# Performance work log

Measured on AMD Instinct MI355X. Metric: run time of the kernel, lower is better.

## Reference

```python
import math
import jax, jax.numpy as jnp
import numpy as np

B, N1, N2 = 4, 1024, 768
DIM, H, DK = 1536, 8, 64
DV = DIM // H          # 192
NRPF = DIM // H        # 192, divisible by 6
ESM_CELL = 1280 + 256  # 1536
LN_EPS = 1e-5


def layer_norm(t, g, b):
    mu = jnp.mean(t, axis=-1, keepdims=True)
    var = jnp.mean(jnp.square(t - mu), axis=-1, keepdims=True)
    return (t - mu) * jax.lax.rsqrt(var + LN_EPS) * g + b


def positional_embed(n, feature_size):
    # Enformer-style relative positional features for distances -n+1..n-1
    distances = jnp.arange(-n + 1, n, dtype=jnp.float32)  # [2n-1]
    absd = jnp.abs(distances)[:, None]
    nb = feature_size // 6  # 3 basis fns x 2 (sym + signed)
    seq_len = float(n)
    # exponential
    max_range = math.log(seq_len) / math.log(2.0)
    half_life = 2.0 ** jnp.linspace(3.0, max_range, nb)
    f_exp = jnp.exp(-math.log(2.0) / half_life * absd)
    # central mask
    widths = 2.0 ** jnp.arange(1, nb + 1, dtype=jnp.float32) - 1.0
    f_cm = (widths[None, :] > absd).astype(jnp.float32)
    # gamma pdf
    stddev = seq_len / (2.0 * nb)
    start_mean = seq_len / nb
    mean = jnp.linspace(start_mean, seq_len, nb)
    conc = (mean / stddev) ** 2
    rate = mean / stddev ** 2
    log_p = jax.scipy.special.xlogy(conc - 1.0, absd) - rate * absd
    log_norm = jax.scipy.special.gammaln(conc) - conc * jnp.log(rate)
    prob = jnp.exp(log_p - log_norm) + 1e-8
    f_gam = prob / jnp.max(prob, axis=-1, keepdims=True)
    emb = jnp.concatenate([f_exp, f_cm, f_gam], axis=-1)
    return jnp.concatenate([emb, jnp.sign(distances)[:, None] * emb], axis=-1)  # [2n-1, feature_size]


def relative_shift(x):
    # x: [b, h, t1, 2n-1] -> [b, h, t1, n]
    b, h, t1, _ = x.shape
    x = jnp.pad(x, ((0, 0), (0, 0), (0, 0), (1, 0)))
    t2 = x.shape[-1]  # 2n
    x = x.reshape(b, h, t2, t1)[:, :, 1:, :].reshape(b, h, t1, t2 - 1)
    return x[..., : (t2 + 1) // 2]


def ffn(t, g, b, w1, b1, w2, b2):
    h = layer_norm(t, g, b)
    h = jax.nn.relu(h @ w1 + b1)
    return h @ w2 + b2


def setup_inputs() -> dict:
    key = jax.random.key(0)
    ks = jax.random.split(key, 20)
    s = 0.02
    d = {
        'x': jax.random.normal(ks[0], (B, N1, DIM), jnp.float32),
        'y0': jax.random.normal(ks[1], (B, N2, ESM_CELL), jnp.float32),
        'res_w': jax.random.normal(ks[2], (ESM_CELL, DIM)) * s,
        'lnx_g': jnp.ones((DIM,)), 'lnx_b': jnp.zeros((DIM,)),
        'lny_g': jnp.ones((DIM,)), 'lny_b': jnp.zeros((DIM,)),
        'wq': jax.random.normal(ks[3], (DIM, H * DK)) * s,
        'wk': jax.random.normal(ks[4], (DIM, H * DK)) * s,
        'wv1': jax.random.normal(ks[5], (DIM, H * DV)) * s,
        'wv2': jax.random.normal(ks[6], (DIM, H * DV)) * s,
        'wrel': jax.random.normal(ks[7], (NRPF, H * DK)) * s,
        'rel_pos_bias': jax.random.normal(ks[8], (1, H, 1, DK)),
        'wo1': jax.random.normal(ks[9], (H * DV, DIM)) * s, 'bo1': jnp.zeros((DIM,)),
        'wo2': jax.random.normal(ks[10], (H * DV, DIM)) * s, 'bo2': jnp.zeros((DIM,)),
        'fx_ln_g': jnp.ones((DIM,)), 'fx_ln_b': jnp.zeros((DIM,)),
        'fx_w1': jax.random.normal(ks[11], (DIM, 2 * DIM)) * s, 'fx_b1': jnp.zeros((2 * DIM,)),
        'fx_w2': jax.random.normal(ks[12], (2 * DIM, DIM)) * s, 'fx_b2': jnp.zeros((DIM,)),
        'fy_ln_g': jnp.ones((DIM,)), 'fy_ln_b': jnp.zeros((DIM,)),
        'fy_w1': jax.random.normal(ks[13], (DIM, 2 * DIM)) * s, 'fy_b1': jnp.zeros((2 * DIM,)),
        'fy_w2': jax.random.normal(ks[14], (2 * DIM, DIM)) * s, 'fy_b2': jnp.zeros((DIM,)),
    }
    return d


def reference(x, y0, res_w, lnx_g, lnx_b, lny_g, lny_b, wq, wk, wv1, wv2,
              wrel, rel_pos_bias, wo1, bo1, wo2, bo2,
              fx_ln_g, fx_ln_b, fx_w1, fx_b1, fx_w2, fx_b2,
              fy_ln_g, fy_ln_b, fy_w1, fy_b1, fy_w2, fy_b2):
    scale = DK ** -0.5
    y = y0 @ res_w                                   # res_proj (first layer)
    x1 = layer_norm(x, lnx_g, lnx_b)
    y1 = layer_norm(y, lny_g, lny_b)

    def heads(t, dh):  # [b, n, h*dh] -> [b, h, n, dh]
        return t.reshape(t.shape[0], t.shape[1], H, dh).transpose(0, 2, 1, 3)

    q = heads(x1 @ wq, DK) * scale                   # [b,h,n1,dk]
    k = heads(y1 @ wk, DK)                           # [b,h,n2,dk]
    v2 = heads(y1 @ wv2, DV)                         # [b,h,n2,dv]

    content = jnp.einsum('bhid,bhjd->bhij', q, k)    # [b,h,n1,n2]

    pos = positional_embed(N1, NRPF)                 # [2n1-1, nrpf]
    rel_q = (pos @ wrel).reshape(2 * N1 - 1, H, DK).transpose(1, 0, 2)  # [h,2n1-1,dk]
    rel_logits = jnp.einsum('bhjd,hnd->bhjn', k * scale + rel_pos_bias, rel_q)  # [b,h,n2,2n1-1]
    rel_logits = relative_shift(rel_logits)          # [b,h,n2,n1]
    logits = content + rel_logits.transpose(0, 1, 3, 2)

    attn = jax.nn.softmax(logits, axis=-1)           # [b,h,n1,n2]

    out1 = jnp.einsum('bhij,bhjd->bhid', attn, v2)   # [b,h,n1,dv]
    out1 = out1.transpose(0, 2, 1, 3).reshape(B, N1, H * DV)
    x2 = out1 @ wo1 + bo1

    # exchange branch: reuse attn^T on v1 from stream x
    v1 = heads(x1 @ wv1, DV)                         # [b,h,n1,dv]
    out2 = jnp.einsum('bhij,bhid->bhjd', attn, v1)   # [b,h,n2,dv]
    out2 = out2.transpose(0, 2, 1, 3).reshape(B, N2, H * DV)
    y2 = out2 @ wo2 + bo2

    x4 = x + x2
    x5 = x4 + ffn(x4, fx_ln_g, fx_ln_b, fx_w1, fx_b1, fx_w2, fx_b2)
    y4 = y + y2
    y5 = y4 + ffn(y4, fy_ln_g, fy_ln_b, fy_w1, fy_b1, fy_w2, fy_b2)
    return x5, y5
```

## Files before the change

kernel.cpp:

```cpp
#include <hip/hip_runtime.h>
#include <stdint.h>
#include <math.h>

typedef __attribute__((ext_vector_type(8))) short s8v;
typedef __attribute__((ext_vector_type(4))) short s4v;
typedef __attribute__((ext_vector_type(4))) float f4v;

#define DEV static __device__ __forceinline__

DEV short f2bf(float f) {
  uint32_t u = __builtin_bit_cast(uint32_t, f);
  u += 0x7FFFu + ((u >> 16) & 1u);
  return (short)(u >> 16);
}
DEV float bf2f(short s) {
  uint32_t u = ((uint32_t)(uint16_t)s) << 16;
  return __builtin_bit_cast(float, u);
}

#define GLD16(g, l) __builtin_amdgcn_global_load_lds( \
    (const __attribute__((address_space(1))) void*)(g), \
    (__attribute__((address_space(3))) void*)(l), 16, 0, 0)

__global__ __launch_bounds__(256) void gemm_bt(
    const short* __restrict__ A, const short* __restrict__ B,
    float* Cf, short* Cb,
    const float* __restrict__ bias, const float* resid,
    int M, int N, int K, int lda, int ldb, int ldc,
    long long sAo, long long sAi, long long sBo, long long sBi,
    long long sCo, long long sCi, float alpha, int relu)
{
  __shared__ __align__(16) short lA[128*32];
  __shared__ __align__(16) short lB[128*32];
  const int z = blockIdx.z, zo = z >> 3, zi = z & 7;
  const short* Ab = A + zo*sAo + zi*sAi;
  const short* Bb = B + zo*sBo + zi*sBi;
  const long long cOff = zo*sCo + zi*sCi;

  const int m0 = blockIdx.y*128, n0 = blockIdx.x*128;
  const int tid = threadIdx.x, lane = tid & 63, wv = tid >> 6;
  const int wm = (wv >> 1)*64, wn = (wv & 1)*64;
  const int fr = lane & 15, fq = lane >> 4;

  f4v acc[4][4] = {};

  const int rA0 = min(m0 + (tid >> 2), M - 1);
  const int rA1 = min(m0 + 64 + (tid >> 2), M - 1);
  const int rB0 = min(n0 + (tid >> 2), N - 1);
  const int rB1 = min(n0 + 64 + (tid >> 2), N - 1);
  const int pc = (tid & 3) * 8;
  const short* gA0 = Ab + (size_t)rA0*lda + pc;
  const short* gA1 = Ab + (size_t)rA1*lda + pc;
  const short* gB0 = Bb + (size_t)rB0*ldb + pc;
  const short* gB1 = Bb + (size_t)rB1*ldb + pc;
  short* dA0 = lA + (wv*64)*8;
  short* dA1 = lA + (256 + wv*64)*8;
  short* dB0 = lB + (wv*64)*8;
  short* dB1 = lB + (256 + wv*64)*8;

  for (int k0 = 0; k0 < K; k0 += 32) {
    GLD16(gA0 + k0, dA0);
    GLD16(gA1 + k0, dA1);
    GLD16(gB0 + k0, dB0);
    GLD16(gB1 + k0, dB1);
    __syncthreads();
    s8v af[4], bg[4];
#pragma unroll
    for (int i = 0; i < 4; i++) {
      af[i] = *(const s8v*)&lA[(wm + i*16 + fr)*32 + fq*8];
      bg[i] = *(const s8v*)&lB[(wn + i*16 + fr)*32 + fq*8];
    }
#pragma unroll
    for (int mi = 0; mi < 4; mi++)
#pragma unroll
      for (int ni = 0; ni < 4; ni++)
        acc[mi][ni] = __builtin_amdgcn_mfma_f32_16x16x32_bf16(af[mi], bg[ni], acc[mi][ni], 0, 0, 0);
    __syncthreads();
  }

#pragma unroll
  for (int mi = 0; mi < 4; mi++) {
    const int row = m0 + wm + mi*16 + fq*4;
#pragma unroll
    for (int ni = 0; ni < 4; ni++) {
      const int col = n0 + wn + ni*16 + fr;
      if (col >= N) continue;
      const float bv = bias ? bias[col] : 0.f;
#pragma unroll
      for (int r = 0; r < 4; r++) {
        if (row + r >= M) continue;
        float v = acc[mi][ni][r] * alpha + bv;
        const long long idx = cOff + (long long)(row + r)*ldc + col;
        if (resid) v += resid[idx];
        if (relu) v = fmaxf(v, 0.f);
        if (Cf) Cf[idx] = v;
        if (Cb) Cb[idx] = f2bf(v);
      }
    }
  }
}

#define ST_A(buf, ks, tt) do { const int ko = ((tt)<<6) + ((ks)<<5); \
    GLD16(gA0 + ko, ldA + ((buf)*2+(ks))*8192); \
    GLD16(gA1 + ko, ldA + ((buf)*2+(ks))*8192 + 4096); } while(0)
#define ST_B(buf, ks, tt) do { const int ko = ((tt)<<6) + ((ks)<<5); \
    GLD16(gB0 + ko, ldB + ((buf)*2+(ks))*8192); \
    GLD16(gB1 + ko, ldB + ((buf)*2+(ks))*8192 + 4096); } while(0)

#define PH256(buf, ks, mig, READB, DOWAIT, ...) do { \
    s8v av[4]; \
    const int rb = ((buf)*2+(ks))*8192; \
    _Pragma("unroll") for (int q2 = 0; q2 < 4; q2++) av[q2] = *(const s8v*)&smem[rb + aoff[(mig)*4+q2]]; \
    if (READB) { _Pragma("unroll") for (int q2 = 0; q2 < 4; q2++) bv[q2] = *(const s8v*)&smem[32768 + rb + boff[q2]]; } \
    __VA_ARGS__; \
    if (DOWAIT == 1) asm volatile("s_waitcnt vmcnt(6)" ::: "memory"); \
    if (DOWAIT == 2) asm volatile("s_waitcnt vmcnt(0)" ::: "memory"); \
    __builtin_amdgcn_s_barrier(); \
    asm volatile("s_waitcnt lgkmcnt(0)" ::: "memory"); \
    __builtin_amdgcn_sched_barrier(0); \
    __builtin_amdgcn_s_setprio(1); \
    _Pragma("unroll") for (int q2 = 0; q2 < 4; q2++) \
      _Pragma("unroll") for (int u2 = 0; u2 < 4; u2++) \
        acc[(mig)*4+q2][u2] = __builtin_amdgcn_mfma_f32_16x16x32_bf16(av[q2], bv[u2], acc[(mig)*4+q2][u2], 0, 0, 0); \
    __builtin_amdgcn_s_setprio(0); \
    __builtin_amdgcn_s_barrier(); \
    asm volatile("" ::: "memory"); \
  } while(0)

__global__ __launch_bounds__(512, 2) void gemm256(
    const short* __restrict__ A0p, const short* __restrict__ B0p,
    float* C0f, short* C0b, const float* __restrict__ bias0, const float* res0,
    int nb0, int nbm0, int N0, float al0,
    const short* __restrict__ A1p, const short* __restrict__ B1p,
    float* C1f, short* C1b, const float* __restrict__ bias1, const float* res1,
    int nb01, int nbm1, int N1, float al1,
    const short* __restrict__ A2p, const short* __restrict__ B2p,
    float* C2f, short* C2b, const float* __restrict__ bias2, const float* res2,
    int nbm2, int N2, float al2,
    int K, int relu)
{
  __shared__ __align__(16) short smem[65536];
  const int total = gridDim.x;
  int bid = blockIdx.x;
  if ((total & 7) == 0) bid = (bid & 7)*(total >> 3) + (bid >> 3);
  const short* A; const short* B; float* Cf; short* Cb; const float* bias; const float* resid;
  int tile, nbm, N; float alpha;
  if (bid < nb0)       { A = A0p; B = B0p; Cf = C0f; Cb = C0b; bias = bias0; resid = res0;
                         tile = bid; nbm = nbm0; N = N0; alpha = al0; }
  else if (bid < nb01) { A = A1p; B = B1p; Cf = C1f; Cb = C1b; bias = bias1; resid = res1;
                         tile = bid - nb0; nbm = nbm1; N = N1; alpha = al1; }
  else                 { A = A2p; B = B2p; Cf = C2f; Cb = C2b; bias = bias2; resid = res2;
                         tile = bid - nb01; nbm = nbm2; N = N2; alpha = al2; }
  const int bm = tile % nbm, bn = tile / nbm;
  const int m0 = bm << 8, n0 = bn << 8;
  const int t = threadIdx.x, lane = t & 63, w = t >> 6;
  const int wm = w >> 2, wn = w & 3;
  const int fr = lane & 15, fq = lane >> 4;
  const int ntk = K >> 6;

  const int r0 = t >> 2, r1 = 128 + (t >> 2), gsw = t & 3;
  const int cs0 = (gsw ^ ((r0 >> 1) & 3)) << 3;
  const int cs1 = (gsw ^ ((r1 >> 1) & 3)) << 3;
  const short* gA0 = A + (size_t)(m0 + r0)*K + cs0;
  const short* gA1 = A + (size_t)(m0 + r1)*K + cs1;
  const short* gB0 = B + (size_t)(n0 + r0)*K + cs0;
  const short* gB1 = B + (size_t)(n0 + r1)*K + cs1;
  short* const ldA = smem + w*512;
  short* const ldB = smem + 32768 + w*512;

  int aoff[8], boff[4];
#pragma unroll
  for (int mi = 0; mi < 8; mi++) { const int r = wm*128 + mi*16 + fr; aoff[mi] = r*32 + ((fq ^ ((r >> 1) & 3)) << 3); }
#pragma unroll
  for (int ni = 0; ni < 4; ni++) { const int r = wn*64 + ni*16 + fr; boff[ni] = r*32 + ((fq ^ ((r >> 1) & 3)) << 3); }

  f4v acc[8][4] = {};
  s8v bv[4];

  ST_A(0,0,0); ST_B(0,0,0); ST_A(0,1,0); ST_B(0,1,0);
  ST_B(1,0,1); ST_A(1,0,1); ST_B(1,1,1);
  asm volatile("s_waitcnt vmcnt(6)" ::: "memory");
  __builtin_amdgcn_s_barrier();
  asm volatile("" ::: "memory");

  for (int it = 0, nit = (ntk >> 1) - 1; it < nit; ++it) {
    const int t1 = 2*it + 1, t2 = 2*it + 2, t3 = 2*it + 3;
    PH256(0,0,0, 1,0, ST_A(1,1,t1));
    PH256(0,0,1, 0,0, ST_B(0,0,t2));
    PH256(0,1,0, 1,0, ST_A(0,0,t2));
    PH256(0,1,1, 0,1, ST_B(0,1,t2));
    PH256(1,0,0, 1,0, ST_A(0,1,t2));
    PH256(1,0,1, 0,0, ST_B(1,0,t3));
    PH256(1,1,0, 1,0, ST_A(1,0,t3));
    PH256(1,1,1, 0,1, ST_B(1,1,t3));
  }
  PH256(0,0,0, 1,0, ST_A(1,1,ntk-1));
  PH256(0,0,1, 0,0, );
  PH256(0,1,0, 1,0, );
  PH256(0,1,1, 0,2, );
  PH256(1,0,0, 1,0, );
  PH256(1,0,1, 0,0, );
  PH256(1,1,0, 1,0, );
  PH256(1,1,1, 0,0, );

#pragma unroll
  for (int mi = 0; mi < 8; mi++) {
    const int row = m0 + wm*128 + mi*16 + fq*4;
#pragma unroll
    for (int ni = 0; ni < 4; ni++) {
      const int col = n0 + wn*64 + ni*16 + fr;
      const float bvv = bias ? bias[col] : 0.f;
#pragma unroll
      for (int r = 0; r < 4; r++) {
        float v = acc[mi][ni][r]*alpha + bvv;
        const size_t idx = (size_t)(row + r)*N + col;
        if (resid) v += resid[idx];
        if (relu) v = fmaxf(v, 0.f);
        if (Cf) Cf[idx] = v;
        else Cb[idx] = f2bf(v);
      }
    }
  }
}

__global__ __launch_bounds__(256) void wtrans(const float* __restrict__ src,
                                              short* __restrict__ dst, int R, int C)
{
  __shared__ float t[32][33];
  const int c0 = blockIdx.x*32, r0 = blockIdx.y*32;
  const int tx = threadIdx.x, ty = threadIdx.y;
#pragma unroll
  for (int k = 0; k < 4; k++)
    t[ty + k*8][tx] = src[(size_t)(r0 + ty + k*8)*C + c0 + tx];
  __syncthreads();
#pragma unroll
  for (int k = 0; k < 4; k++)
    dst[(size_t)(c0 + ty + k*8)*R + r0 + tx] = f2bf(t[tx][ty + k*8]);
}

__global__ __launch_bounds__(256) void btrans(const short* __restrict__ src, short* __restrict__ dst,
    int ls, int ld_, long long sSo, long long sSi, long long sDo, long long sDi)
{
  __shared__ short t[32][33];
  const int z = blockIdx.z;
  const short* S = src + (z>>3)*sSo + (z&7)*sSi;
  short* D = dst + (z>>3)*sDo + (z&7)*sDi;
  const int c0 = blockIdx.x*32, r0 = blockIdx.y*32;
  const int tx = threadIdx.x, ty = threadIdx.y;
#pragma unroll
  for (int k = 0; k < 4; k++)
    t[ty + k*8][tx] = S[(size_t)(r0 + ty + k*8)*ls + c0 + tx];
  __syncthreads();
#pragma unroll
  for (int k = 0; k < 4; k++)
    D[(size_t)(c0 + ty + k*8)*ld_ + r0 + tx] = t[tx][ty + k*8];
}

__global__ __launch_bounds__(256) void conv_bf(const float* __restrict__ src,
                                               short* __restrict__ dst, long long n)
{
  const long long i = ((long long)blockIdx.x*256 + threadIdx.x)*4;
  if (i >= n) return;
  const float4 v = *(const float4*)(src + i);
  s4v o = { f2bf(v.x), f2bf(v.y), f2bf(v.z), f2bf(v.w) };
  *(s4v*)(dst + i) = o;
}

__global__ __launch_bounds__(256) void ln_k(const float* __restrict__ in,
    const float* __restrict__ gam, const float* __restrict__ bet, short* __restrict__ out)
{
  const long long row = blockIdx.x;
  const float* r = in + row*1536;
  const int tid = threadIdx.x;
  float v[6], s = 0.f, s2 = 0.f;
#pragma unroll
  for (int i = 0; i < 6; i++) { v[i] = r[tid + i*256]; s += v[i]; s2 += v[i]*v[i]; }
  for (int m = 1; m < 64; m <<= 1) { s += __shfl_xor(s, m); s2 += __shfl_xor(s2, m); }
  __shared__ float rs[4], rs2[4];
  if ((tid & 63) == 0) { rs[tid>>6] = s; rs2[tid>>6] = s2; }
  __syncthreads();
  s = rs[0]+rs[1]+rs[2]+rs[3]; s2 = rs2[0]+rs2[1]+rs2[2]+rs2[3];
  const float mu  = s * (1.f/1536.f);
  const float var = s2 * (1.f/1536.f) - mu*mu;
  const float inv = rsqrtf(var + 1e-5f);
  short* o = out + row*1536;
#pragma unroll
  for (int i = 0; i < 6; i++) { int c = tid + i*256; o[c] = f2bf((v[i]-mu)*inv*gam[c] + bet[c]); }
}

__global__ __launch_bounds__(64) void posemb(short* __restrict__ out)
{
  const int i = blockIdx.x;
  const int j = threadIdx.x;
  const float dist = (float)(i - 1023);
  const float absd = fabsf(dist);
  float fe = 0.f, fc = 0.f, prob = 0.f;
  if (j < 32) {
    const float hl = exp2f(3.f + 7.f*(float)j/31.f);
    fe = expf(-0.6931471805599453f/hl * absd);
    const float width = exp2f((float)(j+1)) - 1.f;
    fc = (width > absd) ? 1.f : 0.f;
    const float m = 32.f*(float)(j+1);
    const float conc = (m/16.f)*(m/16.f);
    const float rate = m/256.f;
    const float logp = (absd > 0.f ? (conc-1.f)*logf(absd) : -INFINITY) - rate*absd;
    const float logn = lgammaf(conc) - conc*logf(rate);
    prob = expf(logp - logn) + 1e-8f;
  }
  float mx = prob;
  for (int m = 1; m < 32; m <<= 1) mx = fmaxf(mx, __shfl_xor(mx, m));
  if (j < 32) {
    const float fg = prob / mx;
    const float sg = dist > 0.f ? 1.f : (dist < 0.f ? -1.f : 0.f);
    const size_t base = (size_t)i*192;
    out[base + j]       = f2bf(fe);
    out[base + 32 + j]  = f2bf(fc);
    out[base + 64 + j]  = f2bf(fg);
    out[base + 96 + j]  = f2bf(sg*fe);
    out[base + 128 + j] = f2bf(sg*fc);
    out[base + 160 + j] = f2bf(sg*fg);
  }
}

__global__ __launch_bounds__(256) void relbias_k(const float* __restrict__ rpb,
    const short* __restrict__ relq, float* __restrict__ T)
{
  const int n = blockIdx.x;
  const int tid = threadIdx.x;
  const int h = tid >> 5, l = tid & 31;
  const int d = l*2;
  float s = rpb[h*64+d]   * bf2f(relq[(size_t)n*512 + h*64 + d])
          + rpb[h*64+d+1] * bf2f(relq[(size_t)n*512 + h*64 + d+1]);
  for (int m = 1; m < 32; m <<= 1) s += __shfl_xor(s, m);
  if (l == 0) T[h*2047 + n] = s;
}

__global__ __launch_bounds__(256) void scores_k(
    const short* __restrict__ qb, const short* __restrict__ kb,
    const short* __restrict__ relq, const float* __restrict__ T,
    float* __restrict__ L)
{
  __shared__ __align__(16) short smem[21504];
  short* kt  = smem;
  short* qt  = smem + 4608;
  short* rqt = smem + 4608;
  float* P   = (float*)(smem + 4608);

  const int z = blockIdx.z, b = z >> 3, h = z & 7;
  const int j0 = blockIdx.x*64, i0 = blockIdx.y*64;
  const int tid = threadIdx.x, lane = tid & 63, wv = tid >> 6;
  const int fr = lane & 15, fq = lane >> 4;

  {
    const short* kg = kb + (size_t)(b*768  + j0)*512 + h*64;
    const short* qg = qb + (size_t)(b*1024 + i0)*512 + h*64;
    for (int c = tid; c < 512; c += 256) {
      const int r = c >> 3, ch = (c & 7)*8;
      *(s8v*)&kt[r*72 + ch] = *(const s8v*)&kg[(size_t)r*512 + ch];
      *(s8v*)&qt[r*72 + ch] = *(const s8v*)&qg[(size_t)r*512 + ch];
    }
  }
  __syncthreads();

  const int wi = (wv & 1)*32, wj = (wv >> 1)*32;
  f4v c2[2][2] = {};
#pragma unroll
  for (int ks = 0; ks < 2; ks++) {
    s8v aq[2], bk[2];
#pragma unroll
    for (int mi = 0; mi < 2; mi++) aq[mi] = *(const s8v*)&qt[(wi + mi*16 + fr)*72 + ks*32 + fq*8];
#pragma unroll
    for (int ni = 0; ni < 2; ni++) bk[ni] = *(const s8v*)&kt[(wj + ni*16 + fr)*72 + ks*32 + fq*8];
#pragma unroll
    for (int mi = 0; mi < 2; mi++)
#pragma unroll
      for (int ni = 0; ni < 2; ni++)
        c2[mi][ni] = __builtin_amdgcn_mfma_f32_16x16x32_bf16(aq[mi], bk[ni], c2[mi][ni], 0, 0, 0);
  }
  __syncthreads();

  const int nbase = 704 + i0 - j0;
  {
    const short* rg = relq + (size_t)nbase*512 + h*64;
    for (int c = tid; c < 1024; c += 256) {
      const int r = c >> 3, ch = (c & 7)*8;
      *(s8v*)&rqt[r*72 + ch] = *(const s8v*)&rg[(size_t)r*512 + ch];
    }
  }
  __syncthreads();

  const int wj2 = (wv & 1)*32, wn2 = (wv >> 1)*64;
  f4v pr[2][4] = {};
#pragma unroll
  for (int ks = 0; ks < 2; ks++) {
    s8v a2[2], b2[4];
#pragma unroll
    for (int mi = 0; mi < 2; mi++) a2[mi] = *(const s8v*)&kt[(wj2 + mi*16 + fr)*72 + ks*32 + fq*8];
#pragma unroll
    for (int ni = 0; ni < 4; ni++) b2[ni] = *(const s8v*)&rqt[(wn2 + ni*16 + fr)*72 + ks*32 + fq*8];
#pragma unroll
    for (int mi = 0; mi < 2; mi++)
#pragma unroll
      for (int ni = 0; ni < 4; ni++)
        pr[mi][ni] = __builtin_amdgcn_mfma_f32_16x16x32_bf16(a2[mi], b2[ni], pr[mi][ni], 0, 0, 0);
  }
  __syncthreads();

#pragma unroll
  for (int mi = 0; mi < 2; mi++)
#pragma unroll
    for (int ni = 0; ni < 4; ni++)
#pragma unroll
      for (int r = 0; r < 4; r++)
        P[(wj2 + mi*16 + fq*4 + r)*132 + wn2 + ni*16 + fr] = pr[mi][ni][r];
  __syncthreads();

  const float* Tt = T + h*2047 + nbase;
  float* Lb = L + ((size_t)z*1024 + i0)*768 + j0;
#pragma unroll
  for (int mi = 0; mi < 2; mi++)
#pragma unroll
    for (int ni = 0; ni < 2; ni++)
#pragma unroll
      for (int r = 0; r < 4; r++) {
        const int il = wi + mi*16 + fq*4 + r;
        const int jl = wj + ni*16 + fr;
        const int nl = 63 + il - jl;
        Lb[(size_t)il*768 + jl] = c2[mi][ni][r] + 0.125f*P[jl*132 + nl] + Tt[nl];
      }
}

__global__ __launch_bounds__(256) void softmax_k(const float* __restrict__ L, short* __restrict__ P)
{
  const long long row = blockIdx.x;
  const float* r = L + row*768;
  const int tid = threadIdx.x;
  float v0 = r[tid], v1 = r[tid+256], v2 = r[tid+512];
  float mx = fmaxf(v0, fmaxf(v1, v2));
  for (int m = 1; m < 64; m <<= 1) mx = fmaxf(mx, __shfl_xor(mx, m));
  __shared__ float redm[4], reds[4];
  if ((tid & 63) == 0) redm[tid>>6] = mx;
  __syncthreads();
  mx = fmaxf(fmaxf(redm[0], redm[1]), fmaxf(redm[2], redm[3]));
  v0 = __expf(v0 - mx); v1 = __expf(v1 - mx); v2 = __expf(v2 - mx);
  float s = v0 + v1 + v2;
  for (int m = 1; m < 64; m <<= 1) s += __shfl_xor(s, m);
  if ((tid & 63) == 0) reds[tid>>6] = s;
  __syncthreads();
  s = reds[0] + reds[1] + reds[2] + reds[3];
  const float inv = 1.f / s;
  short* o = P + row*768;
  o[tid] = f2bf(v0*inv); o[tid+256] = f2bf(v1*inv); o[tid+512] = f2bf(v2*inv);
}

static void gemm(hipStream_t st, const short* A, const short* B, float* Cf, short* Cb,
                 const float* bias, const float* resid,
                 int M, int N, int K, int lda, int ldb, int ldc,
                 int batches = 1,
                 long long sAo = 0, long long sAi = 0, long long sBo = 0, long long sBi = 0,
                 long long sCo = 0, long long sCi = 0, float alpha = 1.f, int relu = 0)
{
  dim3 g((N + 127)/128, (M + 127)/128, batches);
  gemm_bt<<<g, dim3(256), 0, st>>>(A, B, Cf, Cb, bias, resid, M, N, K, lda, ldb, ldc,
                                   sAo, sAi, sBo, sBi, sCo, sCi, alpha, relu);
}

static void g256_3(hipStream_t st,
    const short* A0, const short* B0, float* C0f, short* C0b, const float* bias0, const float* res0,
    int M0, int N0, float al0,
    const short* A1, const short* B1, float* C1f, short* C1b, const float* bias1, const float* res1,
    int M1, int N1, float al1,
    const short* A2, const short* B2, float* C2f, short* C2b, const float* bias2, const float* res2,
    int M2, int N2, float al2,
    int K, int relu)
{
  const int nbm0 = M0 >> 8, nb0 = nbm0*(N0 >> 8);
  const int nbm1 = M1 >> 8, nb1 = nbm1*(N1 >> 8);
  const int nbm2 = M2 >> 8, nb2 = M2 ? nbm2*(N2 >> 8) : 0;
  gemm256<<<dim3(nb0 + nb1 + nb2), dim3(512), 0, st>>>(
      A0, B0, C0f, C0b, bias0, res0, nb0, nbm0, N0, al0,
      A1, B1, C1f, C1b, bias1, res1, nb0 + nb1, nbm1, N1, al1,
      A2, B2, C2f, C2b, bias2, res2, nbm2, N2, al2, K, relu);
}

static void g256(hipStream_t st,
    const short* A0, const short* B0, float* C0f, short* C0b, const float* bias0, const float* res0,
    int M0, int N0, float al0,
    const short* A1, const short* B1, float* C1f, short* C1b, const float* bias1, const float* res1,
    int M1, int N1, float al1,
    int K, int relu)
{
  g256_3(st, A0, B0, C0f, C0b, bias0, res0, M0, N0, al0,
         A1, B1, C1f, C1b, bias1, res1, M1, N1, al1,
         nullptr, nullptr, nullptr, nullptr, nullptr, nullptr, 0, 256, 1.f, K, relu);
}

extern "C" void kernel_launch(void* const* d_in, const int* in_sizes, int n_in,
                              void* d_out, int out_size, void* d_ws, size_t ws_size,
                              hipStream_t stream)
{
  (void)in_sizes; (void)n_in; (void)out_size; (void)ws_size;
  const float* x     = (const float*)d_in[0];
  const float* y0    = (const float*)d_in[1];
  const float* lnxg  = (const float*)d_in[3];
  const float* lnxb  = (const float*)d_in[4];
  const float* lnyg  = (const float*)d_in[5];
  const float* lnyb  = (const float*)d_in[6];
  const float* rpb   = (const float*)d_in[12];
  const float* bo1   = (const float*)d_in[14];
  const float* bo2   = (const float*)d_in[16];
  const float* fxg   = (const float*)d_in[17];
  const float* fxbb  = (const float*)d_in[18];
  const float* fxb1  = (const float*)d_in[20];
  const float* fxb2  = (const float*)d_in[22];
  const float* fyg   = (const float*)d_in[23];
  const float* fybb  = (const float*)d_in[24];
  const float* fyb1  = (const float*)d_in[26];
  const float* fyb2  = (const float*)d_in[28];

  char* base = (char*)d_ws;
  size_t off = 0;
  auto bump = [&](size_t b) -> char* { char* p = base + off; off += (b + 255) & ~(size_t)255; return p; };

  short* W_A  = (short*)bump(4718592);
  short* W_B  = (short*)bump(1572864);
  short* W_B2 = (short*)bump(1572864);
  short* W_C  = (short*)bump(4718592);
  short* W_D  = (short*)bump(196608);
  short* W_E  = (short*)bump(9437184);
  short* W_F  = (short*)bump(9437184);

  char*  uB = bump(12582912);  short* x1 = (short*)uB;   short* out1 = (short*)uB;
  char*  uC = bump(9437184);   short* y1 = (short*)uC;   short* out2 = (short*)uC;
  char*  uD = bump(9437184);
  short* y0b = (short*)uD;
  short* qb  = (short*)uD;
  short* kbB = (short*)(uD + 4194304);
  float* Tbl   = (float*)bump(262016);
  short* posb  = (short*)bump(786048);
  short* relqb = (short*)bump(2096128);
  char*  uG = bump(12582912);  short* v1b = (short*)uG;  short* x4ln = (short*)uG;
  char*  uH = bump(9437184);   short* v2b = (short*)uH;  short* y4ln = (short*)uH;
  char*  uI = bump(100663296);
  short* wv2T   = (short*)uI;
  float* logits = (float*)uI;
  short* attnT  = (short*)uI;
  short* v1T    = (short*)(uI + 50331648);
  short* v2T    = (short*)(uI + 62914560);
  short* hx     = (short*)uI;
  short* hy     = (short*)(uI + 25165824);
  short* fy1T   = (short*)(uI + 46137344);
  short* fy2T   = (short*)(uI + 55574528);
  char*  U2 = bump(50331648);
  short* attnb = (short*)U2;
  float* y4    = (float*)U2;

  float* outx = (float*)d_out;
  float* outy = (float*)d_out + 6291456;
  float* x4  = outx;
  float* y_f = outy;

  auto WT = [&](int idx, short* dst, int R, int C) {
    wtrans<<<dim3(C/32, R/32), dim3(32,8), 0, stream>>>((const float*)d_in[idx], dst, R, C);
  };

  WT(2,  W_A, 1536, 1536);
  WT(11, W_D, 192,  512);
  WT(9,  W_C, 1536, 1536);
  WT(10, wv2T, 1536, 1536);
  WT(7,  W_B, 1536, 512);
  WT(8,  W_B2, 1536, 512);
  WT(19, W_E, 1536, 3072);
  WT(21, W_F, 3072, 1536);
  conv_bf<<<4608, 256, 0, stream>>>(y0, y0b, 4718592LL);
  posemb<<<2047, 64, 0, stream>>>(posb);
  gemm(stream, posb, W_D, nullptr, relqb, nullptr, nullptr, 2047, 512, 192, 192, 192, 512);
  relbias_k<<<2047, 256, 0, stream>>>(rpb, relqb, Tbl);
  ln_k<<<4096, 256, 0, stream>>>(x, lnxg, lnxb, x1);
  g256(stream, y0b, W_A, y_f, nullptr, nullptr, nullptr, 3072, 1536, 1.f,
       x1, W_C, nullptr, v1b, nullptr, nullptr, 4096, 1536, 1.f, 1536, 0);
  ln_k<<<3072, 256, 0, stream>>>(y_f, lnyg, lnyb, y1);
  g256_3(stream, y1, wv2T, nullptr, v2b, nullptr, nullptr, 3072, 1536, 1.f,
         x1, W_B, nullptr, qb, nullptr, nullptr, 4096, 512, 0.125f,
         y1, W_B2, nullptr, kbB, nullptr, nullptr, 3072, 512, 1.f, 1536, 0);
  WT(13, W_A, 1536, 1536);
  WT(15, W_C, 1536, 1536);
  scores_k<<<dim3(12,16,32), 256, 0, stream>>>(qb, kbB, relqb, Tbl, logits);
  softmax_k<<<32768, 256, 0, stream>>>(logits, attnb);
  btrans<<<dim3(24,32,32), dim3(32,8), 0, stream>>>(attnb, attnT, 768, 1024,
       8LL*786432, 786432, 8LL*786432, 786432);
  btrans<<<dim3(6,32,32), dim3(32,8), 0, stream>>>(v1b, v1T, 1536, 1024,
       1024LL*1536, 192, 8LL*196608, 196608);
  btrans<<<dim3(6,24,32), dim3(32,8), 0, stream>>>(v2b, v2T, 1536, 768,
       768LL*1536, 192, 8LL*147456, 147456);
  gemm(stream, attnb, v2T, nullptr, out1, nullptr, nullptr, 1024, 192, 768, 768, 768, 1536,
       32, 8LL*786432, 786432, 8LL*147456, 147456, 1024LL*1536, 192);
  gemm(stream, attnT, v1T, nullptr, out2, nullptr, nullptr, 768, 192, 1024, 1024, 1024, 1536,
       32, 8LL*786432, 786432, 8LL*196608, 196608, 768LL*1536, 192);
  WT(25, fy1T, 1536, 3072);
  WT(27, fy2T, 3072, 1536);
  g256(stream, out1, W_A, x4, nullptr, bo1, x, 4096, 1536, 1.f,
       out2, W_C, y4, nullptr, bo2, y_f, 3072, 1536, 1.f, 1536, 0);
  ln_k<<<4096, 256, 0, stream>>>(x4, fxg, fxbb, x4ln);
  ln_k<<<3072, 256, 0, stream>>>(y4, fyg, fybb, y4ln);
  g256(stream, x4ln, W_E, nullptr, hx, fxb1, nullptr, 4096, 3072, 1.f,
       y4ln, fy1T, nullptr, hy, fyb1, nullptr, 3072, 3072, 1.f, 1536, 1);
  g256(stream, hx, W_F, outx, nullptr, fxb2, x4, 4096, 1536, 1.f,
       hy, fy2T, outy, nullptr, fyb2, y4, 3072, 1536, 1.f, 3072, 0);
}
```

Before: 732.7 us.

## Fold weight transposes into tail blocks of the big GEMM launches

Appends extra thread blocks to the gemm256 launches that transpose and convert fp32 weights to bf16 for later stages. Those transposes then run alongside GEMM tiles instead of as separate serial wtrans launches, filling the idle CUs in the last wave and cutting launch count. It also removes the sched_barrier and the trailing s_barrier inside each MFMA phase, letting the compiler interleave more freely at some risk to LDS buffer-reuse safety. Tail blocks add work to the GEMM grid and could delay its completion if scheduled late.

After: 774.3 us. 5.7% more time.

```diff
diff --git a/kernel.cpp b/kernel.cpp
--- a/kernel.cpp
+++ b/kernel.cpp
@@ -21,6 +21,11 @@
 #define GLD16(g, l) __builtin_amdgcn_global_load_lds( \
     (const __attribute__((address_space(1))) void*)(g), \
     (__attribute__((address_space(3))) void*)(l), 16, 0, 0)
+
+struct TailWT {
+  const float* src[7]; short* dst[7];
+  int R[7], C[7], tiles[7];
+};
 
 __global__ __launch_bounds__(256) void gemm_bt(
     const short* __restrict__ A, const short* __restrict__ B,
@@ -117,14 +122,11 @@
     if (DOWAIT == 2) asm volatile("s_waitcnt vmcnt(0)" ::: "memory"); \
     __builtin_amdgcn_s_barrier(); \
     asm volatile("s_waitcnt lgkmcnt(0)" ::: "memory"); \
-    __builtin_amdgcn_sched_barrier(0); \
     __builtin_amdgcn_s_setprio(1); \
     _Pragma("unroll") for (int q2 = 0; q2 < 4; q2++) \
       _Pragma("unroll") for (int u2 = 0; u2 < 4; u2++) \
         acc[(mig)*4+q2][u2] = __builtin_amdgcn_mfma_f32_16x16x32_bf16(av[q2], bv[u2], acc[(mig)*4+q2][u2], 0, 0, 0); \
     __builtin_amdgcn_s_setprio(0); \
-    __builtin_amdgcn_s_barrier(); \
-    asm volatile("" ::: "memory"); \
   } while(0)
 
 __global__ __launch_bounds__(512, 2) void gemm256(
@@ -137,12 +139,49 @@
     const short* __restrict__ A2p, const short* __restrict__ B2p,
     float* C2f, short* C2b, const float* __restrict__ bias2, const float* res2,
     int nbm2, int N2, float al2,
+    int nb012, TailWT tw,
     int K, int relu)
 {
   __shared__ __align__(16) short smem[65536];
   const int total = gridDim.x;
   int bid = blockIdx.x;
   if ((total & 7) == 0) bid = (bid & 7)*(total >> 3) + (bid >> 3);
+  const int t = threadIdx.x;
+
+  if (bid >= nb012) {
+    const int ntb = total - nb012;
+    const int sub = t >> 8, tt2 = t & 255;
+    const int tx = tt2 & 31, ty2 = tt2 >> 5;
+    int pre[7], NT = 0;
+#pragma unroll
+    for (int o = 0; o < 7; o++) { pre[o] = NT; NT += tw.tiles[o]; }
+    float* tl = (float*)smem + sub*(32*33);
+    for (int base = (bid - nb012)*2; base < NT; base += ntb*2) {
+      const int my = base + sub;
+      int op = 6;
+#pragma unroll
+      for (int o = 6; o >= 1; o--) if (my < pre[o]) op = o - 1;
+      const int loc = my - pre[op];
+      const int Cd = tw.C[op], Rd = tw.R[op], ncx = Cd >> 5;
+      const int cx = (loc % ncx) << 5, ry = (loc / ncx) << 5;
+      if (my < NT) {
+        const float* s = tw.src[op];
+#pragma unroll
+        for (int k2 = 0; k2 < 4; k2++)
+          tl[(ty2 + k2*8)*33 + tx] = s[(size_t)(ry + ty2 + k2*8)*Cd + cx + tx];
+      }
+      __syncthreads();
+      if (my < NT) {
+        short* d2 = tw.dst[op];
+#pragma unroll
+        for (int k2 = 0; k2 < 4; k2++)
+          d2[(size_t)(cx + ty2 + k2*8)*Rd + ry + tx] = f2bf(tl[tx*33 + ty2 + k2*8]);
+      }
+      __syncthreads();
+    }
+    return;
+  }
+
   const short* A; const short* B; float* Cf; short* Cb; const float* bias; const float* resid;
   int tile, nbm, N; float alpha;
   if (bid < nb0)       { A = A0p; B = B0p; Cf = C0f; Cb = C0b; bias = bias0; resid = res0;
@@ -153,7 +192,7 @@
                          tile = bid - nb01; nbm = nbm2; N = N2; alpha = al2; }
   const int bm = tile % nbm, bn = tile / nbm;
   const int m0 = bm << 8, n0 = bn << 8;
-  const int t = threadIdx.x, lane = t & 63, w = t >> 6;
+  const int lane = t & 63, w = t >> 6;
   const int wm = w >> 2, wn = w & 3;
   const int fr = lane & 15, fq = lane >> 4;
   const int ntk = K >> 6;
@@ -472,15 +511,19 @@
     int M1, int N1, float al1,
     const short* A2, const short* B2, float* C2f, short* C2b, const float* bias2, const float* res2,
     int M2, int N2, float al2,
-    int K, int relu)
+    int K, int relu, const TailWT* tw = nullptr, int ntail = 0)
 {
   const int nbm0 = M0 >> 8, nb0 = nbm0*(N0 >> 8);
   const int nbm1 = M1 >> 8, nb1 = nbm1*(N1 >> 8);
   const int nbm2 = M2 >> 8, nb2 = M2 ? nbm2*(N2 >> 8) : 0;
-  gemm256<<<dim3(nb0 + nb1 + nb2), dim3(512), 0, st>>>(
+  const int nb012 = nb0 + nb1 + nb2;
+  TailWT tz{};
+  if (tw) tz = *tw;
+  gemm256<<<dim3(nb012 + ntail), dim3(512), 0, st>>>(
       A0, B0, C0f, C0b, bias0, res0, nb0, nbm0, N0, al0,
       A1, B1, C1f, C1b, bias1, res1, nb0 + nb1, nbm1, N1, al1,
-      A2, B2, C2f, C2b, bias2, res2, nbm2, N2, al2, K, relu);
+      A2, B2, C2f, C2b, bias2, res2, nbm2, N2, al2,
+      nb012, tz, K, relu);
 }
 
 static void g256(hipStream_t st,
@@ -488,11 +531,11 @@
     int M0, int N0, float al0,
     const short* A1, const short* B1, float* C1f, short* C1b, const float* bias1, const float* res1,
     int M1, int N1, float al1,
-    int K, int relu)
+    int K, int relu, const TailWT* tw = nullptr, int ntail = 0)
 {
   g256_3(st, A0, B0, C0f, C0b, bias0, res0, M0, N0, al0,
          A1, B1, C1f, C1b, bias1, res1, M1, N1, al1,
-         nullptr, nullptr, nullptr, nullptr, nullptr, nullptr, 0, 256, 1.f, K, relu);
+         nullptr, nullptr, nullptr, nullptr, nullptr, nullptr, 0, 256, 1.f, K, relu, tw, ntail);
 }
 
 extern "C" void kernel_launch(void* const* d_in, const int* in_sizes, int n_in,
@@ -563,28 +606,34 @@
   auto WT = [&](int idx, short* dst, int R, int C) {
     wtrans<<<dim3(C/32, R/32), dim3(32,8), 0, stream>>>((const float*)d_in[idx], dst, R, C);
   };
+  auto setop = [&](TailWT& tw, int i, int idx, short* dst, int R, int C) {
+    tw.src[i] = (const float*)d_in[idx]; tw.dst[i] = dst;
+    tw.R[i] = R; tw.C[i] = C; tw.tiles[i] = (R >> 5)*(C >> 5);
+  };
 
   WT(2,  W_A, 1536, 1536);
+  WT(9,  W_C, 1536, 1536);
   WT(11, W_D, 192,  512);
-  WT(9,  W_C, 1536, 1536);
-  WT(10, wv2T, 1536, 1536);
-  WT(7,  W_B, 1536, 512);
-  WT(8,  W_B2, 1536, 512);
-  WT(19, W_E, 1536, 3072);
-  WT(21, W_F, 3072, 1536);
   conv_bf<<<4608, 256, 0, stream>>>(y0, y0b, 4718592LL);
   posemb<<<2047, 64, 0, stream>>>(posb);
+  ln_k<<<4096, 256, 0, stream>>>(x, lnxg, lnxb, x1);
   gemm(stream, posb, W_D, nullptr, relqb, nullptr, nullptr, 2047, 512, 192, 192, 192, 512);
   relbias_k<<<2047, 256, 0, stream>>>(rpb, relqb, Tbl);
-  ln_k<<<4096, 256, 0, stream>>>(x, lnxg, lnxb, x1);
+  TailWT tA{};
+  setop(tA, 0, 7,  W_B,  1536, 512);
+  setop(tA, 1, 8,  W_B2, 1536, 512);
+  setop(tA, 2, 10, wv2T, 1536, 1536);
+  setop(tA, 3, 19, W_E,  1536, 3072);
+  setop(tA, 4, 21, W_F,  3072, 1536);
   g256(stream, y0b, W_A, y_f, nullptr, nullptr, nullptr, 3072, 1536, 1.f,
-       x1, W_C, nullptr, v1b, nullptr, nullptr, 4096, 1536, 1.f, 1536, 0);
+       x1, W_C, nullptr, v1b, nullptr, nullptr, 4096, 1536, 1.f, 1536, 0, &tA, 88);
   ln_k<<<3072, 256, 0, stream>>>(y_f, lnyg, lnyb, y1);
+  TailWT tB{};
+  setop(tB, 0, 13, W_A, 1536, 1536);
+  setop(tB, 1, 15, W_C, 1536, 1536);
   g256_3(stream, y1, wv2T, nullptr, v2b, nullptr, nullptr, 3072, 1536, 1.f,
          x1, W_B, nullptr, qb, nullptr, nullptr, 4096, 512, 0.125f,
-         y1, W_B2, nullptr, kbB, nullptr, nullptr, 3072, 512, 1.f, 1536, 0);
-  WT(13, W_A, 1536, 1536);
-  WT(15, W_C, 1536, 1536);
+         y1, W_B2, nullptr, kbB, nullptr, nullptr, 3072, 512, 1.f, 1536, 0, &tB, 88);
   scores_k<<<dim3(12,16,32), 256, 0, stream>>>(qb, kbB, relqb, Tbl, logits);
   softmax_k<<<32768, 256, 0, stream>>>(logits, attnb);
   btrans<<<dim3(24,32,32), dim3(32,8), 0, stream>>>(attnb, attnT, 768, 1024,
@@ -597,10 +646,11 @@
        32, 8LL*786432, 786432, 8LL*147456, 147456, 1024LL*1536, 192);
   gemm(stream, attnT, v1T, nullptr, out2, nullptr, nullptr, 768, 192, 1024, 1024, 1024, 1536,
        32, 8LL*786432, 786432, 8LL*196608, 196608, 768LL*1536, 192);
-  WT(25, fy1T, 1536, 3072);
-  WT(27, fy2T, 3072, 1536);
+  TailWT tC{};
+  setop(tC, 0, 25, fy1T, 1536, 3072);
+  setop(tC, 1, 27, fy2T, 3072, 1536);
   g256(stream, out1, W_A, x4, nullptr, bo1, x, 4096, 1536, 1.f,
-       out2, W_C, y4, nullptr, bo2, y_f, 3072, 1536, 1.f, 1536, 0);
+       out2, W_C, y4, nullptr, bo2, y_f, 3072, 1536, 1.f, 1536, 0, &tC, 88);
   ln_k<<<4096, 256, 0, stream>>>(x4, fxg, fxbb, x4ln);
   ln_k<<<3072, 256, 0, stream>>>(y4, fyg, fybb, y4ln);
   g256(stream, x4ln, W_E, nullptr, hx, fxb1, nullptr, 4096, 3072, 1.f,
```
